# Kernel tuning notes

Measured on AMD Instinct MI355X. Metric: run time of the kernel, lower is better.

The kernel has to match this reference:

```python
import jax, jax.numpy as jnp
import numpy as np

WINDOW_SIZE = 7
CHANNELS = 3
C1 = 0.01 ** 2
C2 = 0.03 ** 2


def _gaussian_window():
    # 1D gaussian, sigma=1.5, normalized; outer product -> 2D window
    coords = jnp.arange(WINDOW_SIZE, dtype=jnp.float32) - WINDOW_SIZE // 2
    g = jnp.exp(-coords ** 2 / (2 * 1.5 ** 2))
    g = g / g.sum()
    w2d = g[:, None] * g[None, :]  # [7,7]
    # depthwise kernel [C,1,7,7] (OIHW with feature_group_count=C)
    return jnp.tile(w2d[None, None], (CHANNELS, 1, 1, 1))


def _dwconv(x, window):
    pad = WINDOW_SIZE // 2
    return jax.lax.conv_general_dilated(
        x, window,
        window_strides=(1, 1),
        padding=[(pad, pad), (pad, pad)],
        dimension_numbers=('NCHW', 'OIHW', 'NCHW'),
        feature_group_count=CHANNELS,
    )


def setup_inputs() -> dict:
    key = jax.random.key(0)
    k1, k2 = jax.random.split(key)
    shape = (16, 3, 512, 512)
    enhanced = jax.random.uniform(k1, shape, dtype=jnp.float32)
    target = jax.random.uniform(k2, shape, dtype=jnp.float32)
    return {"enhanced": enhanced, "target": target}


def reference(enhanced, target):
    window = _gaussian_window()
    mu1 = _dwconv(enhanced, window)
    mu2 = _dwconv(target, window)
    mu1_sq = mu1 ** 2
    mu2_sq = mu2 ** 2
    mu1_mu2 = mu1 * mu2
    sigma1_sq = _dwconv(enhanced ** 2, window) - mu1_sq
    sigma2_sq = _dwconv(target ** 2, window) - mu2_sq
    sigma12 = _dwconv(enhanced * target, window) - mu1_mu2
    ssim_map = ((2 * mu1_mu2 + C1) * (2 * sigma12 + C2)) / (
        (mu1_sq + mu2_sq + C1) * (sigma1_sq + sigma2_sq + C2))
    return 1.0 - ssim_map.mean()
```

## Files before the change

kernel.cpp:

```cpp
#include <hip/hip_runtime.h>


#define TILE_W 64
#define TILE_H 16
#define HALO 3
#define IN_H 22
#define H_PAIRS 66
#define IMG_H 512
#define IMG_W 512
#define NPLANES 48
#define NTX 8
#define SSIM_C1 1.0e-4f
#define SSIM_C2 9.0e-4f

static __device__ constexpr float G[7] = {
    0.03663284536f, 0.11128076166f, 0.21674531251f, 0.27068216094f,
    0.21674531251f, 0.11128076166f, 0.03663284536f};

__device__ __forceinline__ float2 pk_fma(const float2 a, const float2 b,
                                         const float2 c) {
  float2 d;
  asm("v_pk_fma_f32 %0, %1, %2, %3" : "=v"(d) : "v"(a), "v"(b), "v"(c));
  return d;
}

__device__ __forceinline__ float4 ld4z(const float* __restrict__ row, int col) {
  if (col >= 0 && col + 3 < IMG_W) {
    return *reinterpret_cast<const float4*>(row + col);
  }
  float4 v;
  v.x = ((unsigned)(col + 0) < IMG_W) ? row[col + 0] : 0.f;
  v.y = ((unsigned)(col + 1) < IMG_W) ? row[col + 1] : 0.f;
  v.z = ((unsigned)(col + 2) < IMG_W) ? row[col + 2] : 0.f;
  v.w = ((unsigned)(col + 3) < IMG_W) ? row[col + 3] : 0.f;
  return v;
}

__device__ __forceinline__ void lds_barrier() {
  __builtin_amdgcn_sched_barrier(0);
  asm volatile("s_waitcnt lgkmcnt(0)" ::: "memory");
  __builtin_amdgcn_s_barrier();
  __builtin_amdgcn_sched_barrier(0);
}

__global__ __launch_bounds__(256, 4) void ssim_row_kernel(
    const float* __restrict__ x, const float* __restrict__ y,
    float* __restrict__ partial) {
  __shared__ __align__(16) float2 hbuf[2][IN_H][H_PAIRS];

  const int tid = threadIdx.x;
  const int ty = blockIdx.x;
  const int plane = blockIdx.y;
  const float* __restrict__ xp = x + (size_t)plane * (IMG_H * IMG_W);
  const float* __restrict__ yp = y + (size_t)plane * (IMG_H * IMG_W);
  const int y0 = ty * TILE_H - HALO;
  const bool edge_y = (ty == 0) | (ty == 31);

  const int hr = tid >> 3;
  const int cg = tid & 7;
  const bool active = tid < IN_H * 8;
  const int gy = y0 + hr;

  float4 px[4], py[4];

  auto load_tile = [&](int tx) {
    const int bcol = tx * TILE_W + 8 * cg - 4;
    const bool edge = edge_y | (tx == 0) | (tx == NTX - 1);
    if (!edge) {
      const float* xr = xp + (size_t)gy * IMG_W + bcol;
      const float* yr = yp + (size_t)gy * IMG_W + bcol;
#pragma unroll
      for (int v = 0; v < 4; ++v) {
        px[v] = *reinterpret_cast<const float4*>(xr + 4 * v);
        py[v] = *reinterpret_cast<const float4*>(yr + 4 * v);
      }
    } else if ((unsigned)gy < IMG_H) {
      const float* xr = xp + (size_t)gy * IMG_W;
      const float* yr = yp + (size_t)gy * IMG_W;
#pragma unroll
      for (int v = 0; v < 4; ++v) {
        px[v] = ld4z(xr, bcol + 4 * v);
        py[v] = ld4z(yr, bcol + 4 * v);
      }
    } else {
      const float4 z = make_float4(0.f, 0.f, 0.f, 0.f);
#pragma unroll
      for (int v = 0; v < 4; ++v) { px[v] = z; py[v] = z; }
    }
  };

  auto h_pass = [&]() {
    const float wx[16] = {px[0].x, px[0].y, px[0].z, px[0].w,
                          px[1].x, px[1].y, px[1].z, px[1].w,
                          px[2].x, px[2].y, px[2].z, px[2].w,
                          px[3].x, px[3].y, px[3].z, px[3].w};
    const float wy[16] = {py[0].x, py[0].y, py[0].z, py[0].w,
                          py[1].x, py[1].y, py[1].z, py[1].w,
                          py[2].x, py[2].y, py[2].z, py[2].w,
                          py[3].x, py[3].y, py[3].z, py[3].w};
    float2 A[8], B[8];
#pragma unroll
    for (int j = 0; j < 8; ++j) {
      A[j] = make_float2(0.f, 0.f);
      B[j] = make_float2(0.f, 0.f);
    }
#pragma unroll
    for (int wi = 1; wi < 15; ++wi) {
      const float xv = wx[wi];
      const float yv = wy[wi];
      const float2 xyp = make_float2(xv, yv);
      const float2 spp = make_float2(fmaf(xv, xv, yv * yv), xv * yv);
#pragma unroll
      for (int j = 0; j < 8; ++j) {
        const int k = wi - 1 - j;
        if (k >= 0 && k < 7) {
          const float2 gk2 = make_float2(G[k], G[k]);
          A[j] = pk_fma(gk2, xyp, A[j]);
          B[j] = pk_fma(gk2, spp, B[j]);
        }
      }
    }
    float4* w0 = reinterpret_cast<float4*>(&hbuf[0][hr][8 * cg]);
    float4* w1 = reinterpret_cast<float4*>(&hbuf[1][hr][8 * cg]);
#pragma unroll
    for (int q = 0; q < 4; ++q) {
      w0[q] = make_float4(A[2 * q].x, A[2 * q].y, A[2 * q + 1].x, A[2 * q + 1].y);
      w1[q] = make_float4(B[2 * q].x, B[2 * q].y, B[2 * q + 1].x, B[2 * q + 1].y);
    }
  };

  const int c = tid & 63;
  const int r0 = (tid >> 6) * 4;
  auto v_pass = [&]() -> float {
    float2 M[4], S4[4];
#pragma unroll
    for (int t = 0; t < 4; ++t) {
      M[t] = make_float2(0.f, 0.f);
      S4[t] = make_float2(0.f, 0.f);
    }
#pragma unroll
    for (int j = 0; j < 10; ++j) {
      const float2 mv = hbuf[0][r0 + j][c];
      const float2 sv = hbuf[1][r0 + j][c];
#pragma unroll
      for (int t = 0; t < 4; ++t) {
        const int k = j - t;
        if (k >= 0 && k < 7) {
          const float2 gk2 = make_float2(G[k], G[k]);
          M[t] = pk_fma(gk2, mv, M[t]);
          S4[t] = pk_fma(gk2, sv, S4[t]);
        }
      }
    }
    float a = 0.f;
#pragma unroll
    for (int t = 0; t < 4; ++t) {
      const float mu1 = M[t].x, mu2 = M[t].y;
      const float mu12 = mu1 * mu2;
      const float msq = fmaf(mu1, mu1, mu2 * mu2);
      const float sig12 = S4[t].y - mu12;
      const float sigsum = S4[t].x - msq;
      const float num = fmaf(2.f, mu12, SSIM_C1) * fmaf(2.f, sig12, SSIM_C2);
      const float den = (msq + SSIM_C1) * (sigsum + SSIM_C2);
      float r = __builtin_amdgcn_rcpf(den);
      r = r * fmaf(-den, r, 2.f);
      a = fmaf(num, r, a);
    }
    return a;
  };

  float acc = 0.f;
  if (active) load_tile(0);
#pragma unroll 2
  for (int q = 0; q < NTX; ++q) {
    if (active) {
      h_pass();
      if (q < NTX - 1) load_tile(q + 1);
    }
    lds_barrier();
    acc += v_pass();
    lds_barrier();
  }

#pragma unroll
  for (int off = 32; off > 0; off >>= 1) acc += __shfl_down(acc, off, 64);
  __shared__ float wsum[4];
  if ((tid & 63) == 0) wsum[tid >> 6] = acc;
  __syncthreads();
  if (tid == 0) {
    partial[(size_t)plane * 32 + ty] = wsum[0] + wsum[1] + wsum[2] + wsum[3];
  }
}

__global__ __launch_bounds__(1024) void ssim_reduce_kernel(
    const float* __restrict__ partial, int n, float* __restrict__ out) {
  float acc = 0.f;
  const int nv = n >> 2;
  const float4* __restrict__ p4 = reinterpret_cast<const float4*>(partial);
  for (int i = threadIdx.x; i < nv; i += 1024) {
    const float4 v = p4[i];
    acc += (v.x + v.y) + (v.z + v.w);
  }
#pragma unroll
  for (int off = 32; off > 0; off >>= 1) acc += __shfl_down(acc, off, 64);
  __shared__ float wsum[16];
  if ((threadIdx.x & 63) == 0) wsum[threadIdx.x >> 6] = acc;
  __syncthreads();
  if (threadIdx.x == 0) {
    float s = 0.f;
#pragma unroll
    for (int w = 0; w < 16; ++w) s += wsum[w];
    out[0] = 1.f - s * (1.f / (float)(NPLANES * IMG_H * IMG_W));
  }
}

extern "C" void kernel_launch(void* const* d_in, const int* in_sizes, int n_in,
                              void* d_out, int out_size, void* d_ws, size_t ws_size,
                              hipStream_t stream) {
  const float* enhanced = (const float*)d_in[0];
  const float* target = (const float*)d_in[1];
  float* out = (float*)d_out;
  float* partial = (float*)d_ws;

  dim3 grid(IMG_H / TILE_H, NPLANES, 1);
  dim3 block(256, 1, 1);
  ssim_row_kernel<<<grid, block, 0, stream>>>(enhanced, target, partial);

  const int nblocks = (IMG_H / TILE_H) * NPLANES;
  ssim_reduce_kernel<<<1, 1024, 0, stream>>>(partial, nblocks, out);
}
```

Baseline: 143.8 us.

## Interleave LDS row buffer with XOR swizzle and fuse final reduction via atomics

```diff
diff --git a/kernel.cpp b/kernel.cpp
--- a/kernel.cpp
+++ b/kernel.cpp
@@ -5,11 +5,12 @@
 #define TILE_H 16
 #define HALO 3
 #define IN_H 22
-#define H_PAIRS 66
+#define ROW_SLOTS 66
 #define IMG_H 512
 #define IMG_W 512
 #define NPLANES 48
 #define NTX 8
+#define NB_TOTAL (32 * NPLANES)
 #define SSIM_C1 1.0e-4f
 #define SSIM_C2 9.0e-4f
 
@@ -45,8 +46,8 @@
 
 __global__ __launch_bounds__(256, 4) void ssim_row_kernel(
     const float* __restrict__ x, const float* __restrict__ y,
-    float* __restrict__ partial) {
-  __shared__ __align__(16) float2 hbuf[2][IN_H][H_PAIRS];
+    float* __restrict__ ws, float* __restrict__ out) {
+  __shared__ __align__(16) float4 hbuf[IN_H][ROW_SLOTS];
 
   const int tid = threadIdx.x;
   const int ty = blockIdx.x;
@@ -120,18 +121,20 @@
         }
       }
     }
-    float4* w0 = reinterpret_cast<float4*>(&hbuf[0][hr][8 * cg]);
-    float4* w1 = reinterpret_cast<float4*>(&hbuf[1][hr][8 * cg]);
-#pragma unroll
-    for (int q = 0; q < 4; ++q) {
-      w0[q] = make_float4(A[2 * q].x, A[2 * q].y, A[2 * q + 1].x, A[2 * q + 1].y);
-      w1[q] = make_float4(B[2 * q].x, B[2 * q].y, B[2 * q + 1].x, B[2 * q + 1].y);
+    char* wbase = reinterpret_cast<char*>(&hbuf[hr][cg * 8]);
+    const int cgx = cg << 4;
+#pragma unroll
+    for (int j = 0; j < 8; ++j) {
+      *reinterpret_cast<float4*>(wbase + ((j << 4) ^ cgx)) =
+          make_float4(A[j].x, A[j].y, B[j].x, B[j].y);
     }
   };
 
   const int c = tid & 63;
+  const int slotc = c ^ ((c >> 3) & 7);
   const int r0 = (tid >> 6) * 4;
   auto v_pass = [&]() -> float {
+    const float4* hb = &hbuf[r0][slotc];
     float2 M[4], S4[4];
 #pragma unroll
     for (int t = 0; t < 4; ++t) {
@@ -140,8 +143,9 @@
     }
 #pragma unroll
     for (int j = 0; j < 10; ++j) {
-      const float2 mv = hbuf[0][r0 + j][c];
-      const float2 sv = hbuf[1][r0 + j][c];
+      const float4 v = hb[j * ROW_SLOTS];
+      const float2 mv = make_float2(v.x, v.y);
+      const float2 sv = make_float2(v.z, v.w);
 #pragma unroll
       for (int t = 0; t < 4; ++t) {
         const int k = j - t;
@@ -188,29 +192,16 @@
   if ((tid & 63) == 0) wsum[tid >> 6] = acc;
   __syncthreads();
   if (tid == 0) {
-    partial[(size_t)plane * 32 + ty] = wsum[0] + wsum[1] + wsum[2] + wsum[3];
-  }
-}
-
-__global__ __launch_bounds__(1024) void ssim_reduce_kernel(
-    const float* __restrict__ partial, int n, float* __restrict__ out) {
-  float acc = 0.f;
-  const int nv = n >> 2;
-  const float4* __restrict__ p4 = reinterpret_cast<const float4*>(partial);
-  for (int i = threadIdx.x; i < nv; i += 1024) {
-    const float4 v = p4[i];
-    acc += (v.x + v.y) + (v.z + v.w);
-  }
-#pragma unroll
-  for (int off = 32; off > 0; off >>= 1) acc += __shfl_down(acc, off, 64);
-  __shared__ float wsum[16];
-  if ((threadIdx.x & 63) == 0) wsum[threadIdx.x >> 6] = acc;
-  __syncthreads();
-  if (threadIdx.x == 0) {
-    float s = 0.f;
-#pragma unroll
-    for (int w = 0; w < 16; ++w) s += wsum[w];
-    out[0] = 1.f - s * (1.f / (float)(NPLANES * IMG_H * IMG_W));
+    const float s = wsum[0] + wsum[1] + wsum[2] + wsum[3];
+    atomicAdd(&ws[0], s);
+    __threadfence();
+    const unsigned prev =
+        atomicAdd(reinterpret_cast<unsigned*>(ws) + 1, 1u);
+    if (prev == NB_TOTAL - 1) {
+      __threadfence();
+      const float tot = atomicAdd(&ws[0], 0.0f);
+      out[0] = 1.f - tot * (1.f / (float)(NPLANES * IMG_H * IMG_W));
+    }
   }
 }
 
@@ -220,12 +211,10 @@
   const float* enhanced = (const float*)d_in[0];
   const float* target = (const float*)d_in[1];
   float* out = (float*)d_out;
-  float* partial = (float*)d_ws;
-
+  float* ws = (float*)d_ws;
+
+  hipMemsetAsync(d_ws, 0, 8, stream);
   dim3 grid(IMG_H / TILE_H, NPLANES, 1);
   dim3 block(256, 1, 1);
-  ssim_row_kernel<<<grid, block, 0, stream>>>(enhanced, target, partial);
-
-  const int nblocks = (IMG_H / TILE_H) * NPLANES;
-  ssim_reduce_kernel<<<1, 1024, 0, stream>>>(partial, nblocks, out);
-}
+  ssim_row_kernel<<<grid, block, 0, stream>>>(enhanced, target, ws, out);
+}
```

New measurement: 201.0 us. +39.8%, slower.
